# Performance work log

Measured on AMD Instinct MI355X. Metric: run time of the kernel, lower is better.

Reference implementation:

```python
import jax, jax.numpy as jnp
import numpy as np

# DeepSeek-V3 MoE config (matches init_kwargs)
H = 1024          # hidden_size
I = 704           # moe_intermediate_size
E = 64            # n_routed_experts
TOP_K = 8         # num_experts_per_tok
NG = 8            # n_group
TOPK_GROUP = 4    # topk_group
N_SHARED = 2      # n_shared_experts
ROUTED_SCALE = 2.5
S_I = I * N_SHARED  # shared expert intermediate size


def setup_inputs() -> dict:
    key = jax.random.key(0)
    ks = jax.random.split(key, 10)
    sc = 0.02
    return {
        "hidden_states": jax.random.normal(ks[0], (1, 1024, H), dtype=jnp.float32),
        "gate_w": sc * jax.random.normal(ks[1], (E, H), dtype=jnp.float32),
        "gate_bias": sc * jax.random.normal(ks[2], (E,), dtype=jnp.float32),  # e_score_correction_bias
        "Wg": sc * jax.random.normal(ks[3], (E, I, H), dtype=jnp.float32),
        "Wu": sc * jax.random.normal(ks[4], (E, I, H), dtype=jnp.float32),
        "Wd": sc * jax.random.normal(ks[5], (E, H, I), dtype=jnp.float32),
        "Sg": sc * jax.random.normal(ks[6], (S_I, H), dtype=jnp.float32),
        "Su": sc * jax.random.normal(ks[7], (S_I, H), dtype=jnp.float32),
        "Sd": sc * jax.random.normal(ks[8], (H, S_I), dtype=jnp.float32),
    }


def _route(x, gate_w, gate_bias):
    # x: [T, H] -> dense routing weight matrix [T, E]
    T = x.shape[0]
    logits = x @ gate_w.T                         # [T, E] (fp32, as HF casts to float32)
    scores = jax.nn.sigmoid(logits)
    scores_for_choice = scores + gate_bias[None, :]
    # group scores: sum of top-2 expert scores in each group
    grp = scores_for_choice.reshape(T, NG, E // NG)
    group_scores = jnp.sum(jax.lax.top_k(grp, 2)[0], axis=-1)      # [T, NG]
    _, gidx = jax.lax.top_k(group_scores, TOPK_GROUP)              # [T, TOPK_GROUP]
    gmask = jnp.zeros((T, NG), dtype=scores.dtype).at[
        jnp.arange(T)[:, None], gidx].set(1.0)                      # [T, NG]
    emask = jnp.repeat(gmask, E // NG, axis=1)                      # [T, E]
    masked = jnp.where(emask > 0, scores_for_choice, 0.0)
    _, topk_idx = jax.lax.top_k(masked, TOP_K)                      # [T, TOP_K]
    topk_w = jnp.take_along_axis(scores, topk_idx, axis=1)          # gather from UNbiased scores
    topk_w = topk_w / (jnp.sum(topk_w, axis=-1, keepdims=True) + 1e-20)  # norm_topk_prob
    topk_w = topk_w * ROUTED_SCALE
    # dense [T, E] combine weights (zeros for unrouted experts)
    rw = jnp.zeros((T, E), dtype=scores.dtype).at[
        jnp.arange(T)[:, None], topk_idx].add(topk_w)
    return rw


def _mlp(x, gw, uw, dw):
    # SwiGLU MLP: down(silu(gate(x)) * up(x)), no biases
    return (jax.nn.silu(x @ gw.T) * (x @ uw.T)) @ dw.T


def reference(hidden_states, gate_w, gate_bias, Wg, Wu, Wd, Sg, Su, Sd):
    B, S, _ = hidden_states.shape
    x = hidden_states.reshape(B * S, H)                 # [T, H]
    rw = _route(x, gate_w, gate_bias)                   # [T, E]
    # dense reference: run every expert on every token, weighted combine
    expert_out = jax.vmap(lambda gw_, uw_, dw_: _mlp(x, gw_, uw_, dw_))(Wg, Wu, Wd)  # [E, T, H]
    routed = jnp.einsum('eth,te->th', expert_out, rw)   # [T, H]
    shared = _mlp(x, Sg, Su, Sd)                        # [T, H]
    out = (routed + shared).reshape(B, S, H)
    return out
```

## Files before the change

### kernel.cpp

```cpp
#include <hip/hip_runtime.h>
#include <hip/hip_bf16.h>
#include <cstdint>
#include <cstddef>

#define T_TOK 1024
#define H_DIM 1024
#define I_DIM 704
#define E_NUM 64
#define TOPK 8
#define NGRP 8
#define GSIZE 8
#define TOPKG 4
#define SI_DIM 1408
#define RSCALE 2.5f
#define NSLOT (T_TOK * TOPK)

#define AP 72

typedef short bf16x8 __attribute__((ext_vector_type(8)));
typedef float f32x4 __attribute__((ext_vector_type(4)));

__device__ inline unsigned pk2(float x, float y) {
    __hip_bfloat162 h2 = __float22bfloat162_rn(make_float2(x, y));
    unsigned u; __builtin_memcpy(&u, &h2, 4); return u;
}
__device__ inline unsigned short bf1(float x) {
    __hip_bfloat16 h = __float2bfloat16(x);
    unsigned short u; __builtin_memcpy(&u, &h, 2); return u;
}

__global__ __launch_bounds__(64) void route_kernel(
    const float* __restrict__ x, const float* __restrict__ gw, const float* __restrict__ gb,
    int* __restrict__ counts, int* __restrict__ tk_idx, float* __restrict__ tk_w)
{
    const int t = blockIdx.x;
    __shared__ float xs[H_DIM];
    __shared__ float raw[E_NUM];
    __shared__ float sc[E_NUM];
    __shared__ float masked[E_NUM];
    __shared__ float gsc[NGRP];
    const int tid = threadIdx.x;

    const float4* xrow = (const float4*)(x + (size_t)t * H_DIM);
    for (int i = tid; i < H_DIM / 4; i += 64) ((float4*)xs)[i] = xrow[i];
    __syncthreads();

    float a = 0.f;
    const float* w = gw + (size_t)tid * H_DIM;
    for (int h = 0; h < H_DIM; h += 4) {
        float4 w4 = *(const float4*)(w + h);
        a += xs[h] * w4.x + xs[h+1] * w4.y + xs[h+2] * w4.z + xs[h+3] * w4.w;
    }
    float s = 1.f / (1.f + expf(-a));
    raw[tid] = s;
    sc[tid] = s + gb[tid];
    __syncthreads();

    if (tid == 0) {
        for (int g = 0; g < NGRP; ++g) {
            float m1 = -1e30f, m2 = -1e30f;
            for (int j = 0; j < GSIZE; ++j) {
                float v = sc[g * GSIZE + j];
                if (v > m1) { m2 = m1; m1 = v; }
                else if (v > m2) { m2 = v; }
            }
            gsc[g] = m1 + m2;
        }
        bool gsel[NGRP];
        for (int g = 0; g < NGRP; ++g) gsel[g] = false;
        for (int k = 0; k < TOPKG; ++k) {
            int best = -1; float bv = -1e30f;
            for (int g = 0; g < NGRP; ++g)
                if (!gsel[g] && gsc[g] > bv) { bv = gsc[g]; best = g; }
            gsel[best] = true;
        }
        for (int e = 0; e < E_NUM; ++e)
            masked[e] = gsel[e / GSIZE] ? sc[e] : 0.0f;
        int idx[TOPK];
        float wsum = 0.f;
        for (int k = 0; k < TOPK; ++k) {
            int best = 0; float bv = -1e30f;
            for (int e = 0; e < E_NUM; ++e)
                if (masked[e] > bv) { bv = masked[e]; best = e; }
            masked[best] = -1e30f;
            idx[k] = best;
            wsum += raw[best];
        }
        float inv = RSCALE / (wsum + 1e-20f);
        for (int k = 0; k < TOPK; ++k) {
            tk_idx[t * TOPK + k] = idx[k];
            tk_w[t * TOPK + k] = raw[idx[k]] * inv;
            atomicAdd(&counts[idx[k]], 1);
        }
    }
}

__global__ void zero_kernel(int* counts, int* fillc)
{
    int i = threadIdx.x;
    if (i < E_NUM) { counts[i] = 0; fillc[i] = 0; }
}

__global__ void scan_kernel(const int* __restrict__ counts, int* __restrict__ offs)
{
    if (threadIdx.x == 0) {
        int acc = 0;
        for (int e = 0; e < E_NUM; ++e) { offs[e] = acc; acc += counts[e]; }
    }
}

__global__ void fill_kernel(const int* __restrict__ tk_idx, const float* __restrict__ tk_w,
                            const int* __restrict__ offs, int* __restrict__ fillc,
                            int* __restrict__ tok_list, float* __restrict__ w_list)
{
    int t = blockIdx.x * blockDim.x + threadIdx.x;
    if (t >= T_TOK) return;
    for (int k = 0; k < TOPK; ++k) {
        int e = tk_idx[t * TOPK + k];
        int pos = offs[e] + atomicAdd(&fillc[e], 1);
        tok_list[pos] = t;
        w_list[pos] = tk_w[t * TOPK + k];
    }
}

__global__ __launch_bounds__(256) void gateup_routed_mfma(
    const float* __restrict__ x, const float* __restrict__ Wg, const float* __restrict__ Wu,
    const int* __restrict__ offs, const int* __restrict__ counts,
    const int* __restrict__ tok_list, const float* __restrict__ w_list,
    unsigned short* __restrict__ act)
{
    const int e = blockIdx.z;
    const int cnt = counts[e];
    const int m0 = blockIdx.y * 128;
    if (m0 >= cnt) return;
    const int off = offs[e];
    const int n0 = blockIdx.x * 64;

    __shared__ unsigned short As[128 * AP];
    __shared__ unsigned short Bg[64 * AP];
    __shared__ unsigned short Bu[64 * AP];
    __shared__ int toks[128];
    __shared__ float wts[128];

    const int tid = threadIdx.x;
    if (tid < 128) {
        int s = m0 + tid;
        toks[tid] = (s < cnt) ? tok_list[off + s] : -1;
        wts[tid]  = (s < cnt) ? w_list[off + s] : 0.f;
    }
    __syncthreads();

    const int lane = tid & 63;
    const int wv = tid >> 6;
    const int lr = lane & 15;
    const int lq = lane >> 4;

    f32x4 accg[2][4], accu[2][4];
    #pragma unroll
    for (int i = 0; i < 2; ++i)
        #pragma unroll
        for (int j = 0; j < 4; ++j) {
            accg[i][j] = (f32x4){0.f, 0.f, 0.f, 0.f};
            accu[i][j] = (f32x4){0.f, 0.f, 0.f, 0.f};
        }

    const float* wgp = Wg + (size_t)e * I_DIM * H_DIM + (size_t)n0 * H_DIM;
    const float* wup = Wu + (size_t)e * I_DIM * H_DIM + (size_t)n0 * H_DIM;

    const int ar = tid >> 4;
    const int ac = (tid & 15) * 4;

    for (int k0 = 0; k0 < H_DIM; k0 += 64) {
        #pragma unroll
        for (int p = 0; p < 8; ++p) {
            int r = ar + p * 16;
            int tkn = toks[r];
            float4 v = make_float4(0.f, 0.f, 0.f, 0.f);
            if (tkn >= 0) v = *(const float4*)(x + (size_t)tkn * H_DIM + k0 + ac);
            *(uint2*)&As[r * AP + ac] = make_uint2(pk2(v.x, v.y), pk2(v.z, v.w));
        }
        #pragma unroll
        for (int p = 0; p < 4; ++p) {
            int r = ar + p * 16;
            float4 g = *(const float4*)(wgp + (size_t)r * H_DIM + k0 + ac);
            *(uint2*)&Bg[r * AP + ac] = make_uint2(pk2(g.x, g.y), pk2(g.z, g.w));
            float4 u = *(const float4*)(wup + (size_t)r * H_DIM + k0 + ac);
            *(uint2*)&Bu[r * AP + ac] = make_uint2(pk2(u.x, u.y), pk2(u.z, u.w));
        }
        __syncthreads();
        #pragma unroll
        for (int ks = 0; ks < 2; ++ks) {
            bf16x8 a0 = *(const bf16x8*)&As[(wv * 32 + lr) * AP + ks * 32 + lq * 8];
            bf16x8 a1 = *(const bf16x8*)&As[(wv * 32 + 16 + lr) * AP + ks * 32 + lq * 8];
            #pragma unroll
            for (int nj = 0; nj < 4; ++nj) {
                bf16x8 bg = *(const bf16x8*)&Bg[(nj * 16 + lr) * AP + ks * 32 + lq * 8];
                bf16x8 bu = *(const bf16x8*)&Bu[(nj * 16 + lr) * AP + ks * 32 + lq * 8];
                accg[0][nj] = __builtin_amdgcn_mfma_f32_16x16x32_bf16(a0, bg, accg[0][nj], 0, 0, 0);
                accg[1][nj] = __builtin_amdgcn_mfma_f32_16x16x32_bf16(a1, bg, accg[1][nj], 0, 0, 0);
                accu[0][nj] = __builtin_amdgcn_mfma_f32_16x16x32_bf16(a0, bu, accu[0][nj], 0, 0, 0);
                accu[1][nj] = __builtin_amdgcn_mfma_f32_16x16x32_bf16(a1, bu, accu[1][nj], 0, 0, 0);
            }
        }
        __syncthreads();
    }

    #pragma unroll
    for (int mi = 0; mi < 2; ++mi) {
        #pragma unroll
        for (int r = 0; r < 4; ++r) {
            int srow = wv * 32 + mi * 16 + lq * 4 + r;
            if (m0 + srow < cnt) {
                float w = wts[srow];
                unsigned short* ap = act + (size_t)(off + m0 + srow) * I_DIM + n0 + lr;
                #pragma unroll
                for (int nj = 0; nj < 4; ++nj) {
                    float g = accg[mi][nj][r];
                    float u = accu[mi][nj][r];
                    float a = w * (g / (1.f + __expf(-g))) * u;
                    ap[nj * 16] = bf1(a);
                }
            }
        }
    }
}

__global__ __launch_bounds__(256) void down_routed_mfma(
    const unsigned short* __restrict__ act, const float* __restrict__ Wd,
    const int* __restrict__ offs, const int* __restrict__ counts,
    const int* __restrict__ tok_list, float* __restrict__ out)
{
    const int e = blockIdx.z;
    const int cnt = counts[e];
    const int m0 = blockIdx.y * 128;
    if (m0 >= cnt) return;
    const int off = offs[e];
    const int n0 = blockIdx.x * 64;

    __shared__ unsigned short As[128 * AP];
    __shared__ unsigned short Bs[64 * AP];
    __shared__ int toks[128];

    const int tid = threadIdx.x;
    if (tid < 128) {
        int s = m0 + tid;
        toks[tid] = (s < cnt) ? tok_list[off + s] : 0;
    }
    __syncthreads();

    const int lane = tid & 63;
    const int wv = tid >> 6;
    const int lr = lane & 15;
    const int lq = lane >> 4;

    f32x4 acc[2][4];
    #pragma unroll
    for (int i = 0; i < 2; ++i)
        #pragma unroll
        for (int j = 0; j < 4; ++j)
            acc[i][j] = (f32x4){0.f, 0.f, 0.f, 0.f};

    const float* wdp = Wd + (size_t)e * H_DIM * I_DIM + (size_t)n0 * I_DIM;
    const unsigned short* ap0 = act + (size_t)(off + m0) * I_DIM;
    const int ar = tid >> 4;
    const int ac = (tid & 15) * 4;

    for (int k0 = 0; k0 < I_DIM; k0 += 64) {
        #pragma unroll
        for (int p = 0; p < 8; ++p) {
            int r = ar + p * 16;
            uint2 v = make_uint2(0u, 0u);
            if (m0 + r < cnt) v = *(const uint2*)(ap0 + (size_t)r * I_DIM + k0 + ac);
            *(uint2*)&As[r * AP + ac] = v;
        }
        #pragma unroll
        for (int p = 0; p < 4; ++p) {
            int r = ar + p * 16;
            float4 w4 = *(const float4*)(wdp + (size_t)r * I_DIM + k0 + ac);
            *(uint2*)&Bs[r * AP + ac] = make_uint2(pk2(w4.x, w4.y), pk2(w4.z, w4.w));
        }
        __syncthreads();
        #pragma unroll
        for (int ks = 0; ks < 2; ++ks) {
            bf16x8 a0 = *(const bf16x8*)&As[(wv * 32 + lr) * AP + ks * 32 + lq * 8];
            bf16x8 a1 = *(const bf16x8*)&As[(wv * 32 + 16 + lr) * AP + ks * 32 + lq * 8];
            #pragma unroll
            for (int nj = 0; nj < 4; ++nj) {
                bf16x8 b = *(const bf16x8*)&Bs[(nj * 16 + lr) * AP + ks * 32 + lq * 8];
                acc[0][nj] = __builtin_amdgcn_mfma_f32_16x16x32_bf16(a0, b, acc[0][nj], 0, 0, 0);
                acc[1][nj] = __builtin_amdgcn_mfma_f32_16x16x32_bf16(a1, b, acc[1][nj], 0, 0, 0);
            }
        }
        __syncthreads();
    }

    #pragma unroll
    for (int mi = 0; mi < 2; ++mi) {
        #pragma unroll
        for (int r = 0; r < 4; ++r) {
            int srow = wv * 32 + mi * 16 + lq * 4 + r;
            if (m0 + srow < cnt) {
                int t = toks[srow];
                float* op = out + (size_t)t * H_DIM + n0 + lr;
                #pragma unroll
                for (int nj = 0; nj < 4; ++nj)
                    atomicAdd(&op[nj * 16], acc[mi][nj][r]);
            }
        }
    }
}

__global__ __launch_bounds__(256) void gateup_shared_mfma(
    const float* __restrict__ x, const float* __restrict__ Sg, const float* __restrict__ Su,
    unsigned short* __restrict__ sact)
{
    const int m0 = blockIdx.y * 128;
    const int n0 = blockIdx.x * 64;

    __shared__ unsigned short As[128 * AP];
    __shared__ unsigned short Bg[64 * AP];
    __shared__ unsigned short Bu[64 * AP];

    const int tid = threadIdx.x;
    const int lane = tid & 63;
    const int wv = tid >> 6;
    const int lr = lane & 15;
    const int lq = lane >> 4;

    f32x4 accg[2][4], accu[2][4];
    #pragma unroll
    for (int i = 0; i < 2; ++i)
        #pragma unroll
        for (int j = 0; j < 4; ++j) {
            accg[i][j] = (f32x4){0.f, 0.f, 0.f, 0.f};
            accu[i][j] = (f32x4){0.f, 0.f, 0.f, 0.f};
        }

    const float* gp = Sg + (size_t)n0 * H_DIM;
    const float* up = Su + (size_t)n0 * H_DIM;
    const int ar = tid >> 4;
    const int ac = (tid & 15) * 4;

    for (int k0 = 0; k0 < H_DIM; k0 += 64) {
        #pragma unroll
        for (int p = 0; p < 8; ++p) {
            int r = ar + p * 16;
            float4 v = *(const float4*)(x + (size_t)(m0 + r) * H_DIM + k0 + ac);
            *(uint2*)&As[r * AP + ac] = make_uint2(pk2(v.x, v.y), pk2(v.z, v.w));
        }
        #pragma unroll
        for (int p = 0; p < 4; ++p) {
            int r = ar + p * 16;
            float4 g = *(const float4*)(gp + (size_t)r * H_DIM + k0 + ac);
            *(uint2*)&Bg[r * AP + ac] = make_uint2(pk2(g.x, g.y), pk2(g.z, g.w));
            float4 u = *(const float4*)(up + (size_t)r * H_DIM + k0 + ac);
            *(uint2*)&Bu[r * AP + ac] = make_uint2(pk2(u.x, u.y), pk2(u.z, u.w));
        }
        __syncthreads();
        #pragma unroll
        for (int ks = 0; ks < 2; ++ks) {
            bf16x8 a0 = *(const bf16x8*)&As[(wv * 32 + lr) * AP + ks * 32 + lq * 8];
            bf16x8 a1 = *(const bf16x8*)&As[(wv * 32 + 16 + lr) * AP + ks * 32 + lq * 8];
            #pragma unroll
            for (int nj = 0; nj < 4; ++nj) {
                bf16x8 bg = *(const bf16x8*)&Bg[(nj * 16 + lr) * AP + ks * 32 + lq * 8];
                bf16x8 bu = *(const bf16x8*)&Bu[(nj * 16 + lr) * AP + ks * 32 + lq * 8];
                accg[0][nj] = __builtin_amdgcn_mfma_f32_16x16x32_bf16(a0, bg, accg[0][nj], 0, 0, 0);
                accg[1][nj] = __builtin_amdgcn_mfma_f32_16x16x32_bf16(a1, bg, accg[1][nj], 0, 0, 0);
                accu[0][nj] = __builtin_amdgcn_mfma_f32_16x16x32_bf16(a0, bu, accu[0][nj], 0, 0, 0);
                accu[1][nj] = __builtin_amdgcn_mfma_f32_16x16x32_bf16(a1, bu, accu[1][nj], 0, 0, 0);
            }
        }
        __syncthreads();
    }

    #pragma unroll
    for (int mi = 0; mi < 2; ++mi) {
        #pragma unroll
        for (int r = 0; r < 4; ++r) {
            int trow = m0 + wv * 32 + mi * 16 + lq * 4 + r;
            unsigned short* sp = sact + (size_t)trow * SI_DIM + n0 + lr;
            #pragma unroll
            for (int nj = 0; nj < 4; ++nj) {
                float g = accg[mi][nj][r];
                float u = accu[mi][nj][r];
                float a = (g / (1.f + __expf(-g))) * u;
                sp[nj * 16] = bf1(a);
            }
        }
    }
}

__global__ __launch_bounds__(256) void down_shared_mfma(
    const unsigned short* __restrict__ sact, const float* __restrict__ Sd,
    float* __restrict__ out)
{
    const int m0 = blockIdx.y * 128;
    const int n0 = blockIdx.x * 64;

    __shared__ unsigned short As[128 * AP];
    __shared__ unsigned short Bs[64 * AP];

    const int tid = threadIdx.x;
    const int lane = tid & 63;
    const int wv = tid >> 6;
    const int lr = lane & 15;
    const int lq = lane >> 4;

    f32x4 acc[2][4];
    #pragma unroll
    for (int i = 0; i < 2; ++i)
        #pragma unroll
        for (int j = 0; j < 4; ++j)
            acc[i][j] = (f32x4){0.f, 0.f, 0.f, 0.f};

    const float* wp = Sd + (size_t)n0 * SI_DIM;
    const int ar = tid >> 4;
    const int ac = (tid & 15) * 4;

    for (int k0 = 0; k0 < SI_DIM; k0 += 64) {
        #pragma unroll
        for (int p = 0; p < 8; ++p) {
            int r = ar + p * 16;
            uint2 v = *(const uint2*)(sact + (size_t)(m0 + r) * SI_DIM + k0 + ac);
            *(uint2*)&As[r * AP + ac] = v;
        }
        #pragma unroll
        for (int p = 0; p < 4; ++p) {
            int r = ar + p * 16;
            float4 w4 = *(const float4*)(wp + (size_t)r * SI_DIM + k0 + ac);
            *(uint2*)&Bs[r * AP + ac] = make_uint2(pk2(w4.x, w4.y), pk2(w4.z, w4.w));
        }
        __syncthreads();
        #pragma unroll
        for (int ks = 0; ks < 2; ++ks) {
            bf16x8 a0 = *(const bf16x8*)&As[(wv * 32 + lr) * AP + ks * 32 + lq * 8];
            bf16x8 a1 = *(const bf16x8*)&As[(wv * 32 + 16 + lr) * AP + ks * 32 + lq * 8];
            #pragma unroll
            for (int nj = 0; nj < 4; ++nj) {
                bf16x8 b = *(const bf16x8*)&Bs[(nj * 16 + lr) * AP + ks * 32 + lq * 8];
                acc[0][nj] = __builtin_amdgcn_mfma_f32_16x16x32_bf16(a0, b, acc[0][nj], 0, 0, 0);
                acc[1][nj] = __builtin_amdgcn_mfma_f32_16x16x32_bf16(a1, b, acc[1][nj], 0, 0, 0);
            }
        }
        __syncthreads();
    }

    #pragma unroll
    for (int mi = 0; mi < 2; ++mi) {
        #pragma unroll
        for (int r = 0; r < 4; ++r) {
            int trow = m0 + wv * 32 + mi * 16 + lq * 4 + r;
            float* op = out + (size_t)trow * H_DIM + n0 + lr;
            #pragma unroll
            for (int nj = 0; nj < 4; ++nj)
                op[nj * 16] = acc[mi][nj][r];
        }
    }
}

extern "C" void kernel_launch(void* const* d_in, const int* in_sizes, int n_in,
                              void* d_out, int out_size, void* d_ws, size_t ws_size,
                              hipStream_t stream)
{
    const float* x  = (const float*)d_in[0];
    const float* gw = (const float*)d_in[1];
    const float* gb = (const float*)d_in[2];
    const float* Wg = (const float*)d_in[3];
    const float* Wu = (const float*)d_in[4];
    const float* Wd = (const float*)d_in[5];
    const float* Sg = (const float*)d_in[6];
    const float* Su = (const float*)d_in[7];
    const float* Sd = (const float*)d_in[8];
    float* out = (float*)d_out;

    unsigned short* act  = (unsigned short*)d_ws;
    unsigned short* sact = act + (size_t)NSLOT * I_DIM;
    int* counts   = (int*)(sact + (size_t)T_TOK * SI_DIM);
    int* fillc    = counts + 64;
    int* offs     = fillc + 64;
    int* tk_idx   = offs + 64;
    float* tk_w   = (float*)(tk_idx + NSLOT);
    int* tok_list = (int*)(tk_w + NSLOT);
    float* w_list = (float*)(tok_list + NSLOT);

    zero_kernel<<<1, 64, 0, stream>>>(counts, fillc);
    route_kernel<<<T_TOK, 64, 0, stream>>>(x, gw, gb, counts, tk_idx, tk_w);
    scan_kernel<<<1, 64, 0, stream>>>(counts, offs);
    fill_kernel<<<4, 256, 0, stream>>>(tk_idx, tk_w, offs, fillc, tok_list, w_list);

    gateup_routed_mfma<<<dim3(11, 8, 64), 256, 0, stream>>>(x, Wg, Wu, offs, counts, tok_list, w_list, act);
    gateup_shared_mfma<<<dim3(22, 8, 1), 256, 0, stream>>>(x, Sg, Su, sact);
    down_shared_mfma<<<dim3(16, 8, 1), 256, 0, stream>>>(sact, Sd, out);
    down_routed_mfma<<<dim3(16, 8, 64), 256, 0, stream>>>(act, Wd, offs, counts, tok_list, out);
}
```

Before: 842.0 us.

## Pre-convert weights to bf16 and replace atomic down-proj scatter with slot combine

Adds a conversion pass that turns all expert and shared weights plus the activations into bf16 copies in workspace, so the GEMM kernels load 16-byte bf16 vectors instead of converting fp32 on every tile load. Every call converts the full weight set, roughly 200M elements, which is more traffic than the GEMMs themselves read, since each routed weight tile is otherwise read once per active M tile. The routed down projection now writes bf16 per-slot outputs instead of doing float atomicAdd into the output. A new combine kernel then sums the eight slots per token deterministically. This adds a workspace buffer and an extra rounding to bf16 of the routed partial outputs.

New measurement: 887.3 us. 1.05x slower.

```diff
diff --git a/kernel.cpp b/kernel.cpp
--- a/kernel.cpp
+++ b/kernel.cpp
@@ -28,6 +28,21 @@
     __hip_bfloat16 h = __float2bfloat16(x);
     unsigned short u; __builtin_memcpy(&u, &h, 2); return u;
 }
+__device__ inline float bf2f(unsigned short u) {
+    unsigned v = ((unsigned)u) << 16; float f; __builtin_memcpy(&f, &v, 4); return f;
+}
+
+__global__ __launch_bounds__(256) void cvt_kernel(const float* __restrict__ in,
+                                                  unsigned short* __restrict__ out, int n8)
+{
+    int stride = gridDim.x * blockDim.x;
+    for (int i = blockIdx.x * blockDim.x + threadIdx.x; i < n8; i += stride) {
+        float4 a = ((const float4*)in)[2 * i];
+        float4 b = ((const float4*)in)[2 * i + 1];
+        uint4 o = make_uint4(pk2(a.x, a.y), pk2(a.z, a.w), pk2(b.x, b.y), pk2(b.z, b.w));
+        ((uint4*)out)[i] = o;
+    }
+}
 
 __global__ __launch_bounds__(64) void route_kernel(
     const float* __restrict__ x, const float* __restrict__ gw, const float* __restrict__ gb,
@@ -111,7 +126,8 @@
 
 __global__ void fill_kernel(const int* __restrict__ tk_idx, const float* __restrict__ tk_w,
                             const int* __restrict__ offs, int* __restrict__ fillc,
-                            int* __restrict__ tok_list, float* __restrict__ w_list)
+                            int* __restrict__ tok_list, float* __restrict__ w_list,
+                            int* __restrict__ tk_slot)
 {
     int t = blockIdx.x * blockDim.x + threadIdx.x;
     if (t >= T_TOK) return;
@@ -120,11 +136,15 @@
         int pos = offs[e] + atomicAdd(&fillc[e], 1);
         tok_list[pos] = t;
         w_list[pos] = tk_w[t * TOPK + k];
-    }
-}
-
+        tk_slot[t * TOPK + k] = pos;
+    }
+}
+
+template<bool PRE>
 __global__ __launch_bounds__(256) void gateup_routed_mfma(
-    const float* __restrict__ x, const float* __restrict__ Wg, const float* __restrict__ Wu,
+    const float* __restrict__ x, const unsigned short* __restrict__ xb,
+    const float* __restrict__ Wg, const float* __restrict__ Wu,
+    const unsigned short* __restrict__ bWg, const unsigned short* __restrict__ bWu,
     const int* __restrict__ offs, const int* __restrict__ counts,
     const int* __restrict__ tok_list, const float* __restrict__ w_list,
     unsigned short* __restrict__ act)
@@ -136,9 +156,9 @@
     const int off = offs[e];
     const int n0 = blockIdx.x * 64;
 
-    __shared__ unsigned short As[128 * AP];
-    __shared__ unsigned short Bg[64 * AP];
-    __shared__ unsigned short Bu[64 * AP];
+    __shared__ __align__(16) unsigned short As[128 * AP];
+    __shared__ __align__(16) unsigned short Bg[64 * AP];
+    __shared__ __align__(16) unsigned short Bu[64 * AP];
     __shared__ int toks[128];
     __shared__ float wts[128];
 
@@ -164,28 +184,48 @@
             accu[i][j] = (f32x4){0.f, 0.f, 0.f, 0.f};
         }
 
-    const float* wgp = Wg + (size_t)e * I_DIM * H_DIM + (size_t)n0 * H_DIM;
-    const float* wup = Wu + (size_t)e * I_DIM * H_DIM + (size_t)n0 * H_DIM;
-
+    const int cr = tid >> 3;
+    const int cc8 = (tid & 7) * 8;
     const int ar = tid >> 4;
     const int ac = (tid & 15) * 4;
 
     for (int k0 = 0; k0 < H_DIM; k0 += 64) {
-        #pragma unroll
-        for (int p = 0; p < 8; ++p) {
-            int r = ar + p * 16;
-            int tkn = toks[r];
-            float4 v = make_float4(0.f, 0.f, 0.f, 0.f);
-            if (tkn >= 0) v = *(const float4*)(x + (size_t)tkn * H_DIM + k0 + ac);
-            *(uint2*)&As[r * AP + ac] = make_uint2(pk2(v.x, v.y), pk2(v.z, v.w));
-        }
-        #pragma unroll
-        for (int p = 0; p < 4; ++p) {
-            int r = ar + p * 16;
-            float4 g = *(const float4*)(wgp + (size_t)r * H_DIM + k0 + ac);
-            *(uint2*)&Bg[r * AP + ac] = make_uint2(pk2(g.x, g.y), pk2(g.z, g.w));
-            float4 u = *(const float4*)(wup + (size_t)r * H_DIM + k0 + ac);
-            *(uint2*)&Bu[r * AP + ac] = make_uint2(pk2(u.x, u.y), pk2(u.z, u.w));
+        if (PRE) {
+            #pragma unroll
+            for (int p = 0; p < 4; ++p) {
+                int r = cr + p * 32;
+                int tkn = toks[r];
+                uint4 v = make_uint4(0u, 0u, 0u, 0u);
+                if (tkn >= 0) v = *(const uint4*)(xb + (size_t)tkn * H_DIM + k0 + cc8);
+                *(uint4*)&As[r * AP + cc8] = v;
+            }
+            const unsigned short* bg0 = bWg + ((size_t)e * I_DIM + n0) * H_DIM + k0 + cc8;
+            const unsigned short* bu0 = bWu + ((size_t)e * I_DIM + n0) * H_DIM + k0 + cc8;
+            #pragma unroll
+            for (int p = 0; p < 2; ++p) {
+                int r = cr + p * 32;
+                *(uint4*)&Bg[r * AP + cc8] = *(const uint4*)(bg0 + (size_t)r * H_DIM);
+                *(uint4*)&Bu[r * AP + cc8] = *(const uint4*)(bu0 + (size_t)r * H_DIM);
+            }
+        } else {
+            #pragma unroll
+            for (int p = 0; p < 8; ++p) {
+                int r = ar + p * 16;
+                int tkn = toks[r];
+                float4 v = make_float4(0.f, 0.f, 0.f, 0.f);
+                if (tkn >= 0) v = *(const float4*)(x + (size_t)tkn * H_DIM + k0 + ac);
+                *(uint2*)&As[r * AP + ac] = make_uint2(pk2(v.x, v.y), pk2(v.z, v.w));
+            }
+            const float* wgp = Wg + ((size_t)e * I_DIM + n0) * H_DIM;
+            const float* wup = Wu + ((size_t)e * I_DIM + n0) * H_DIM;
+            #pragma unroll
+            for (int p = 0; p < 4; ++p) {
+                int r = ar + p * 16;
+                float4 g = *(const float4*)(wgp + (size_t)r * H_DIM + k0 + ac);
+                *(uint2*)&Bg[r * AP + ac] = make_uint2(pk2(g.x, g.y), pk2(g.z, g.w));
+                float4 u = *(const float4*)(wup + (size_t)r * H_DIM + k0 + ac);
+                *(uint2*)&Bu[r * AP + ac] = make_uint2(pk2(u.x, u.y), pk2(u.z, u.w));
+            }
         }
         __syncthreads();
         #pragma unroll
@@ -225,10 +265,12 @@
     }
 }
 
+template<bool PRE>
 __global__ __launch_bounds__(256) void down_routed_mfma(
-    const unsigned short* __restrict__ act, const float* __restrict__ Wd,
+    const unsigned short* __restrict__ act,
+    const float* __restrict__ Wd, const unsigned short* __restrict__ bWd,
     const int* __restrict__ offs, const int* __restrict__ counts,
-    const int* __restrict__ tok_list, float* __restrict__ out)
+    unsigned short* __restrict__ dslot)
 {
     const int e = blockIdx.z;
     const int cnt = counts[e];
@@ -237,89 +279,8 @@
     const int off = offs[e];
     const int n0 = blockIdx.x * 64;
 
-    __shared__ unsigned short As[128 * AP];
-    __shared__ unsigned short Bs[64 * AP];
-    __shared__ int toks[128];
-
-    const int tid = threadIdx.x;
-    if (tid < 128) {
-        int s = m0 + tid;
-        toks[tid] = (s < cnt) ? tok_list[off + s] : 0;
-    }
-    __syncthreads();
-
-    const int lane = tid & 63;
-    const int wv = tid >> 6;
-    const int lr = lane & 15;
-    const int lq = lane >> 4;
-
-    f32x4 acc[2][4];
-    #pragma unroll
-    for (int i = 0; i < 2; ++i)
-        #pragma unroll
-        for (int j = 0; j < 4; ++j)
-            acc[i][j] = (f32x4){0.f, 0.f, 0.f, 0.f};
-
-    const float* wdp = Wd + (size_t)e * H_DIM * I_DIM + (size_t)n0 * I_DIM;
-    const unsigned short* ap0 = act + (size_t)(off + m0) * I_DIM;
-    const int ar = tid >> 4;
-    const int ac = (tid & 15) * 4;
-
-    for (int k0 = 0; k0 < I_DIM; k0 += 64) {
-        #pragma unroll
-        for (int p = 0; p < 8; ++p) {
-            int r = ar + p * 16;
-            uint2 v = make_uint2(0u, 0u);
-            if (m0 + r < cnt) v = *(const uint2*)(ap0 + (size_t)r * I_DIM + k0 + ac);
-            *(uint2*)&As[r * AP + ac] = v;
-        }
-        #pragma unroll
-        for (int p = 0; p < 4; ++p) {
-            int r = ar + p * 16;
-            float4 w4 = *(const float4*)(wdp + (size_t)r * I_DIM + k0 + ac);
-            *(uint2*)&Bs[r * AP + ac] = make_uint2(pk2(w4.x, w4.y), pk2(w4.z, w4.w));
-        }
-        __syncthreads();
-        #pragma unroll
-        for (int ks = 0; ks < 2; ++ks) {
-            bf16x8 a0 = *(const bf16x8*)&As[(wv * 32 + lr) * AP + ks * 32 + lq * 8];
-            bf16x8 a1 = *(const bf16x8*)&As[(wv * 32 + 16 + lr) * AP + ks * 32 + lq * 8];
-            #pragma unroll
-            for (int nj = 0; nj < 4; ++nj) {
-                bf16x8 b = *(const bf16x8*)&Bs[(nj * 16 + lr) * AP + ks * 32 + lq * 8];
-                acc[0][nj] = __builtin_amdgcn_mfma_f32_16x16x32_bf16(a0, b, acc[0][nj], 0, 0, 0);
-                acc[1][nj] = __builtin_amdgcn_mfma_f32_16x16x32_bf16(a1, b, acc[1][nj], 0, 0, 0);
-            }
-        }
-        __syncthreads();
-    }
-
-    #pragma unroll
-    for (int mi = 0; mi < 2; ++mi) {
-        #pragma unroll
-        for (int r = 0; r < 4; ++r) {
-            int srow = wv * 32 + mi * 16 + lq * 4 + r;
-            if (m0 + srow < cnt) {
-                int t = toks[srow];
-                float* op = out + (size_t)t * H_DIM + n0 + lr;
-                #pragma unroll
-                for (int nj = 0; nj < 4; ++nj)
-                    atomicAdd(&op[nj * 16], acc[mi][nj][r]);
-            }
-        }
-    }
-}
-
-__global__ __launch_bounds__(256) void gateup_shared_mfma(
-    const float* __restrict__ x, const float* __restrict__ Sg, const float* __restrict__ Su,
-    unsigned short* __restrict__ sact)
-{
-    const int m0 = blockIdx.y * 128;
-    const int n0 = blockIdx.x * 64;
-
-    __shared__ unsigned short As[128 * AP];
-    __shared__ unsigned short Bg[64 * AP];
-    __shared__ unsigned short Bu[64 * AP];
+    __shared__ __align__(16) unsigned short As[128 * AP];
+    __shared__ __align__(16) unsigned short Bs[64 * AP];
 
     const int tid = threadIdx.x;
     const int lane = tid & 63;
@@ -327,6 +288,94 @@
     const int lr = lane & 15;
     const int lq = lane >> 4;
 
+    f32x4 acc[2][4];
+    #pragma unroll
+    for (int i = 0; i < 2; ++i)
+        #pragma unroll
+        for (int j = 0; j < 4; ++j)
+            acc[i][j] = (f32x4){0.f, 0.f, 0.f, 0.f};
+
+    const int cr = tid >> 3;
+    const int cc8 = (tid & 7) * 8;
+    const int ar = tid >> 4;
+    const int ac = (tid & 15) * 4;
+
+    const unsigned short* ap0 = act + (size_t)(off + m0) * I_DIM;
+
+    for (int k0 = 0; k0 < I_DIM; k0 += 64) {
+        #pragma unroll
+        for (int p = 0; p < 4; ++p) {
+            int r = cr + p * 32;
+            uint4 v = make_uint4(0u, 0u, 0u, 0u);
+            if (m0 + r < cnt) v = *(const uint4*)(ap0 + (size_t)r * I_DIM + k0 + cc8);
+            *(uint4*)&As[r * AP + cc8] = v;
+        }
+        if (PRE) {
+            const unsigned short* bd0 = bWd + ((size_t)e * H_DIM + n0) * I_DIM + k0 + cc8;
+            #pragma unroll
+            for (int p = 0; p < 2; ++p) {
+                int r = cr + p * 32;
+                *(uint4*)&Bs[r * AP + cc8] = *(const uint4*)(bd0 + (size_t)r * I_DIM);
+            }
+        } else {
+            const float* wdp = Wd + ((size_t)e * H_DIM + n0) * I_DIM;
+            #pragma unroll
+            for (int p = 0; p < 4; ++p) {
+                int r = ar + p * 16;
+                float4 w4 = *(const float4*)(wdp + (size_t)r * I_DIM + k0 + ac);
+                *(uint2*)&Bs[r * AP + ac] = make_uint2(pk2(w4.x, w4.y), pk2(w4.z, w4.w));
+            }
+        }
+        __syncthreads();
+        #pragma unroll
+        for (int ks = 0; ks < 2; ++ks) {
+            bf16x8 a0 = *(const bf16x8*)&As[(wv * 32 + lr) * AP + ks * 32 + lq * 8];
+            bf16x8 a1 = *(const bf16x8*)&As[(wv * 32 + 16 + lr) * AP + ks * 32 + lq * 8];
+            #pragma unroll
+            for (int nj = 0; nj < 4; ++nj) {
+                bf16x8 b = *(const bf16x8*)&Bs[(nj * 16 + lr) * AP + ks * 32 + lq * 8];
+                acc[0][nj] = __builtin_amdgcn_mfma_f32_16x16x32_bf16(a0, b, acc[0][nj], 0, 0, 0);
+                acc[1][nj] = __builtin_amdgcn_mfma_f32_16x16x32_bf16(a1, b, acc[1][nj], 0, 0, 0);
+            }
+        }
+        __syncthreads();
+    }
+
+    #pragma unroll
+    for (int mi = 0; mi < 2; ++mi) {
+        #pragma unroll
+        for (int r = 0; r < 4; ++r) {
+            int srow = wv * 32 + mi * 16 + lq * 4 + r;
+            if (m0 + srow < cnt) {
+                unsigned short* dp = dslot + (size_t)(off + m0 + srow) * H_DIM + n0 + lr;
+                #pragma unroll
+                for (int nj = 0; nj < 4; ++nj)
+                    dp[nj * 16] = bf1(acc[mi][nj][r]);
+            }
+        }
+    }
+}
+
+template<bool PRE>
+__global__ __launch_bounds__(256) void gateup_shared_mfma(
+    const float* __restrict__ x, const unsigned short* __restrict__ xb,
+    const float* __restrict__ Sg, const float* __restrict__ Su,
+    const unsigned short* __restrict__ bSg, const unsigned short* __restrict__ bSu,
+    unsigned short* __restrict__ sact)
+{
+    const int m0 = blockIdx.y * 128;
+    const int n0 = blockIdx.x * 64;
+
+    __shared__ __align__(16) unsigned short As[128 * AP];
+    __shared__ __align__(16) unsigned short Bg[64 * AP];
+    __shared__ __align__(16) unsigned short Bu[64 * AP];
+
+    const int tid = threadIdx.x;
+    const int lane = tid & 63;
+    const int wv = tid >> 6;
+    const int lr = lane & 15;
+    const int lq = lane >> 4;
+
     f32x4 accg[2][4], accu[2][4];
     #pragma unroll
     for (int i = 0; i < 2; ++i)
@@ -336,25 +385,43 @@
             accu[i][j] = (f32x4){0.f, 0.f, 0.f, 0.f};
         }
 
-    const float* gp = Sg + (size_t)n0 * H_DIM;
-    const float* up = Su + (size_t)n0 * H_DIM;
+    const int cr = tid >> 3;
+    const int cc8 = (tid & 7) * 8;
     const int ar = tid >> 4;
     const int ac = (tid & 15) * 4;
 
     for (int k0 = 0; k0 < H_DIM; k0 += 64) {
-        #pragma unroll
-        for (int p = 0; p < 8; ++p) {
-            int r = ar + p * 16;
-            float4 v = *(const float4*)(x + (size_t)(m0 + r) * H_DIM + k0 + ac);
-            *(uint2*)&As[r * AP + ac] = make_uint2(pk2(v.x, v.y), pk2(v.z, v.w));
-        }
-        #pragma unroll
-        for (int p = 0; p < 4; ++p) {
-            int r = ar + p * 16;
-            float4 g = *(const float4*)(gp + (size_t)r * H_DIM + k0 + ac);
-            *(uint2*)&Bg[r * AP + ac] = make_uint2(pk2(g.x, g.y), pk2(g.z, g.w));
-            float4 u = *(const float4*)(up + (size_t)r * H_DIM + k0 + ac);
-            *(uint2*)&Bu[r * AP + ac] = make_uint2(pk2(u.x, u.y), pk2(u.z, u.w));
+        if (PRE) {
+            #pragma unroll
+            for (int p = 0; p < 4; ++p) {
+                int r = cr + p * 32;
+                *(uint4*)&As[r * AP + cc8] = *(const uint4*)(xb + (size_t)(m0 + r) * H_DIM + k0 + cc8);
+            }
+            const unsigned short* bg0 = bSg + (size_t)n0 * H_DIM + k0 + cc8;
+            const unsigned short* bu0 = bSu + (size_t)n0 * H_DIM + k0 + cc8;
+            #pragma unroll
+            for (int p = 0; p < 2; ++p) {
+                int r = cr + p * 32;
+                *(uint4*)&Bg[r * AP + cc8] = *(const uint4*)(bg0 + (size_t)r * H_DIM);
+                *(uint4*)&Bu[r * AP + cc8] = *(const uint4*)(bu0 + (size_t)r * H_DIM);
+            }
+        } else {
+            #pragma unroll
+            for (int p = 0; p < 8; ++p) {
+                int r = ar + p * 16;
+                float4 v = *(const float4*)(x + (size_t)(m0 + r) * H_DIM + k0 + ac);
+                *(uint2*)&As[r * AP + ac] = make_uint2(pk2(v.x, v.y), pk2(v.z, v.w));
+            }
+            const float* gp = Sg + (size_t)n0 * H_DIM;
+            const float* up = Su + (size_t)n0 * H_DIM;
+            #pragma unroll
+            for (int p = 0; p < 4; ++p) {
+                int r = ar + p * 16;
+                float4 g = *(const float4*)(gp + (size_t)r * H_DIM + k0 + ac);
+                *(uint2*)&Bg[r * AP + ac] = make_uint2(pk2(g.x, g.y), pk2(g.z, g.w));
+                float4 u = *(const float4*)(up + (size_t)r * H_DIM + k0 + ac);
+                *(uint2*)&Bu[r * AP + ac] = make_uint2(pk2(u.x, u.y), pk2(u.z, u.w));
+            }
         }
         __syncthreads();
         #pragma unroll
@@ -391,15 +458,17 @@
     }
 }
 
+template<bool PRE>
 __global__ __launch_bounds__(256) void down_shared_mfma(
-    const unsigned short* __restrict__ sact, const float* __restrict__ Sd,
+    const unsigned short* __restrict__ sact,
+    const float* __restrict__ Sd, const unsigned short* __restrict__ bSd,
     float* __restrict__ out)
 {
     const int m0 = blockIdx.y * 128;
     const int n0 = blockIdx.x * 64;
 
-    __shared__ unsigned short As[128 * AP];
-    __shared__ unsigned short Bs[64 * AP];
+    __shared__ __align__(16) unsigned short As[128 * AP];
+    __shared__ __align__(16) unsigned short Bs[64 * AP];
 
     const int tid = threadIdx.x;
     const int lane = tid & 63;
@@ -414,22 +483,32 @@
         for (int j = 0; j < 4; ++j)
             acc[i][j] = (f32x4){0.f, 0.f, 0.f, 0.f};
 
-    const float* wp = Sd + (size_t)n0 * SI_DIM;
+    const int cr = tid >> 3;
+    const int cc8 = (tid & 7) * 8;
     const int ar = tid >> 4;
     const int ac = (tid & 15) * 4;
 
     for (int k0 = 0; k0 < SI_DIM; k0 += 64) {
         #pragma unroll
-        for (int p = 0; p < 8; ++p) {
-            int r = ar + p * 16;
-            uint2 v = *(const uint2*)(sact + (size_t)(m0 + r) * SI_DIM + k0 + ac);
-            *(uint2*)&As[r * AP + ac] = v;
-        }
-        #pragma unroll
         for (int p = 0; p < 4; ++p) {
-            int r = ar + p * 16;
-            float4 w4 = *(const float4*)(wp + (size_t)r * SI_DIM + k0 + ac);
-            *(uint2*)&Bs[r * AP + ac] = make_uint2(pk2(w4.x, w4.y), pk2(w4.z, w4.w));
+            int r = cr + p * 32;
+            *(uint4*)&As[r * AP + cc8] = *(const uint4*)(sact + (size_t)(m0 + r) * SI_DIM + k0 + cc8);
+        }
+        if (PRE) {
+            const unsigned short* bd0 = bSd + (size_t)n0 * SI_DIM + k0 + cc8;
+            #pragma unroll
+            for (int p = 0; p < 2; ++p) {
+                int r = cr + p * 32;
+                *(uint4*)&Bs[r * AP + cc8] = *(const uint4*)(bd0 + (size_t)r * SI_DIM);
+            }
+        } else {
+            const float* wp = Sd + (size_t)n0 * SI_DIM;
+            #pragma unroll
+            for (int p = 0; p < 4; ++p) {
+                int r = ar + p * 16;
+                float4 w4 = *(const float4*)(wp + (size_t)r * SI_DIM + k0 + ac);
+                *(uint2*)&Bs[r * AP + ac] = make_uint2(pk2(w4.x, w4.y), pk2(w4.z, w4.w));
+            }
         }
         __syncthreads();
         #pragma unroll
@@ -457,6 +536,27 @@
                 op[nj * 16] = acc[mi][nj][r];
         }
     }
+}
+
+__global__ __launch_bounds__(256) void combine_kernel(
+    const unsigned short* __restrict__ dslot, const int* __restrict__ tk_slot,
+    float* __restrict__ out)
+{
+    const int t = blockIdx.x;
+    const int c0 = threadIdx.x * 4;
+    int slots[TOPK];
+    #pragma unroll
+    for (int k = 0; k < TOPK; ++k) slots[k] = tk_slot[t * TOPK + k];
+    float4 o = *(float4*)(out + (size_t)t * H_DIM + c0);
+    #pragma unroll
+    for (int k = 0; k < TOPK; ++k) {
+        uint2 v = *(const uint2*)(dslot + (size_t)slots[k] * H_DIM + c0);
+        o.x += bf2f((unsigned short)(v.x & 0xffff));
+        o.y += bf2f((unsigned short)(v.x >> 16));
+        o.z += bf2f((unsigned short)(v.y & 0xffff));
+        o.w += bf2f((unsigned short)(v.y >> 16));
+    }
+    *(float4*)(out + (size_t)t * H_DIM + c0) = o;
 }
 
 extern "C" void kernel_launch(void* const* d_in, const int* in_sizes, int n_in,
@@ -474,23 +574,64 @@
     const float* Sd = (const float*)d_in[8];
     float* out = (float*)d_out;
 
-    unsigned short* act  = (unsigned short*)d_ws;
-    unsigned short* sact = act + (size_t)NSLOT * I_DIM;
-    int* counts   = (int*)(sact + (size_t)T_TOK * SI_DIM);
+    const size_t NW  = (size_t)E_NUM * I_DIM * H_DIM;
+    const size_t NS  = (size_t)SI_DIM * H_DIM;
+    const size_t NX  = (size_t)T_TOK * H_DIM;
+
+    unsigned short* act   = (unsigned short*)d_ws;
+    unsigned short* sact  = act + (size_t)NSLOT * I_DIM;
+    unsigned short* dslot = sact + (size_t)T_TOK * SI_DIM;
+    int* counts   = (int*)(dslot + (size_t)NSLOT * H_DIM);
     int* fillc    = counts + 64;
     int* offs     = fillc + 64;
     int* tk_idx   = offs + 64;
     float* tk_w   = (float*)(tk_idx + NSLOT);
     int* tok_list = (int*)(tk_w + NSLOT);
     float* w_list = (float*)(tok_list + NSLOT);
+    int* tk_slot  = (int*)(w_list + NSLOT);
+    size_t base_end = (size_t)((char*)(tk_slot + NSLOT) - (char*)d_ws);
+    base_end = (base_end + 255) & ~(size_t)255;
+
+    size_t conv_bytes = (3 * NW + 3 * NS + NX) * sizeof(unsigned short);
+    bool pre = (ws_size >= base_end + conv_bytes);
+
+    unsigned short* bWg = (unsigned short*)((char*)d_ws + base_end);
+    unsigned short* bWu = bWg + NW;
+    unsigned short* bWd = bWu + NW;
+    unsigned short* bSg = bWd + NW;
+    unsigned short* bSu = bSg + NS;
+    unsigned short* bSd = bSu + NS;
+    unsigned short* xb  = bSd + NS;
 
     zero_kernel<<<1, 64, 0, stream>>>(counts, fillc);
     route_kernel<<<T_TOK, 64, 0, stream>>>(x, gw, gb, counts, tk_idx, tk_w);
     scan_kernel<<<1, 64, 0, stream>>>(counts, offs);
-    fill_kernel<<<4, 256, 0, stream>>>(tk_idx, tk_w, offs, fillc, tok_list, w_list);
-
-    gateup_routed_mfma<<<dim3(11, 8, 64), 256, 0, stream>>>(x, Wg, Wu, offs, counts, tok_list, w_list, act);
-    gateup_shared_mfma<<<dim3(22, 8, 1), 256, 0, stream>>>(x, Sg, Su, sact);
-    down_shared_mfma<<<dim3(16, 8, 1), 256, 0, stream>>>(sact, Sd, out);
-    down_routed_mfma<<<dim3(16, 8, 64), 256, 0, stream>>>(act, Wd, offs, counts, tok_list, out);
-}
+    fill_kernel<<<4, 256, 0, stream>>>(tk_idx, tk_w, offs, fillc, tok_list, w_list, tk_slot);
+
+    if (pre) {
+        cvt_kernel<<<2048, 256, 0, stream>>>(Wg, bWg, (int)(NW / 8));
+        cvt_kernel<<<2048, 256, 0, stream>>>(Wu, bWu, (int)(NW / 8));
+        cvt_kernel<<<2048, 256, 0, stream>>>(Wd, bWd, (int)(NW / 8));
+        cvt_kernel<<<512, 256, 0, stream>>>(Sg, bSg, (int)(NS / 8));
+        cvt_kernel<<<512, 256, 0, stream>>>(Su, bSu, (int)(NS / 8));
+        cvt_kernel<<<512, 256, 0, stream>>>(Sd, bSd, (int)(NS / 8));
+        cvt_kernel<<<512, 256, 0, stream>>>(x, xb, (int)(NX / 8));
+
+        gateup_routed_mfma<true><<<dim3(11, 8, 64), 256, 0, stream>>>(
+            x, xb, Wg, Wu, bWg, bWu, offs, counts, tok_list, w_list, act);
+        gateup_shared_mfma<true><<<dim3(22, 8, 1), 256, 0, stream>>>(
+            x, xb, Sg, Su, bSg, bSu, sact);
+        down_shared_mfma<true><<<dim3(16, 8, 1), 256, 0, stream>>>(sact, Sd, bSd, out);
+        down_routed_mfma<true><<<dim3(16, 8, 64), 256, 0, stream>>>(
+            act, Wd, bWd, offs, counts, dslot);
+    } else {
+        gateup_routed_mfma<false><<<dim3(11, 8, 64), 256, 0, stream>>>(
+            x, xb, Wg, Wu, bWg, bWu, offs, counts, tok_list, w_list, act);
+        gateup_shared_mfma<false><<<dim3(22, 8, 1), 256, 0, stream>>>(
+            x, xb, Sg, Su, bSg, bSu, sact);
+        down_shared_mfma<false><<<dim3(16, 8, 1), 256, 0, stream>>>(sact, Sd, bSd, out);
+        down_routed_mfma<false><<<dim3(16, 8, 64), 256, 0, stream>>>(
+            act, Wd, bWd, offs, counts, dslot);
+    }
+    combine_kernel<<<T_TOK, 256, 0, stream>>>(dslot, tk_slot, out);
+}
```
